# Kernel tuning notes

Hardware: AMD Instinct MI355X
Metric: run time of the kernel (lower is better)

The kernel has to match this reference:

```python
import jax, jax.numpy as jnp
import numpy as np


def conv1d_same(x, w, b, dilation=1):
    # x: [B, T, Cin], w: [K, Cin, Cout] (WIO), 'same' padding, stride 1
    y = jax.lax.conv_general_dilated(
        x, w, window_strides=(1,), padding='SAME',
        rhs_dilation=(dilation,), dimension_numbers=('NWC', 'WIO', 'NWC'))
    return y + b


def setup_inputs() -> dict:
    key = jax.random.key(0)
    ks = jax.random.split(key, 6)
    B, T, N_IN, N_OUT, ATTN_DIM, KSZ = 16, 2048, 96, 128, 64, 3
    return {
        'x': jax.random.normal(ks[0], (B, T, N_IN), jnp.float32),
        'qkv_w': jax.random.normal(ks[1], (N_IN, 3 * ATTN_DIM), jnp.float32) * 0.05,
        'qkv_b': jnp.zeros((3 * ATTN_DIM,), jnp.float32),
        'scale': jnp.ones((), jnp.float32),
        'conv_w1': jax.random.normal(ks[2], (KSZ, ATTN_DIM, N_OUT), jnp.float32) * 0.05,
        'conv_b1': jnp.zeros((N_OUT,), jnp.float32),
        'conv_w2': jax.random.normal(ks[3], (KSZ, N_OUT, N_OUT), jnp.float32) * 0.05,
        'conv_b2': jnp.zeros((N_OUT,), jnp.float32),
        'down_w': jax.random.normal(ks[4], (N_IN, N_OUT), jnp.float32) * 0.1,
    }


def reference(x, qkv_w, qkv_b, scale, conv_w1, conv_b1, conv_w2, conv_b2, down_w):
    # Dense4Attention: single Dense(3*attn_dim), split into q,k,v
    qkv = x @ qkv_w + qkv_b                       # [B,T,3*D]
    q, k, v = jnp.split(qkv, 3, axis=-1)          # each [B,T,D]
    # AttentionBlock: scores = q k^T * learned scale; non-causal (default)
    scores = jnp.einsum('btd,bsd->bts', q, k) * scale   # [B,T,T]
    weights = jax.nn.softmax(scores, axis=2)            # softmax_axis=2
    out_attn = jnp.einsum('bts,bsd->btd', weights, v)   # [B,T,D]
    h = jax.nn.relu(conv1d_same(out_attn, conv_w1, conv_b1, 1))
    out = jax.nn.relu(conv1d_same(h, conv_w2, conv_b2, 1))   # [B,T,n_out]
    # enhanced residual: softmax over time of row-sums of attn weights
    weight_x = jax.nn.softmax(jnp.sum(weights, axis=2), axis=1)  # [B,T]
    en_res_x = (weight_x[..., None] * x) @ down_w   # n_in != n_out -> downsample
    res = x @ down_w                                 # skip path downsample
    return jax.nn.relu(out + res + en_res_x)
```

## Files before the change

kernel.cpp:

```cpp
#include <hip/hip_runtime.h>
#include <cstdint>

#define B_   16
#define T_   2048
#define CIN  96
#define DH   64
#define NOUT 128

typedef float floatx4 __attribute__((ext_vector_type(4)));
typedef short shortx8 __attribute__((ext_vector_type(8)));
typedef unsigned int uintx2 __attribute__((ext_vector_type(2)));

__device__ __forceinline__ unsigned short f2bf(float f) {
  unsigned int u = __float_as_uint(f);
  u += 0x7FFFu + ((u >> 16) & 1u);
  return (unsigned short)(u >> 16);
}
__device__ __forceinline__ uint32_t cvtpk(float lo, float hi) {
  uint32_t r;
  asm("v_cvt_pk_bf16_f32 %0, %1, %2" : "=v"(r) : "v"(lo), "v"(hi));
  return r;
}
__device__ __forceinline__ floatx4 f4zero() { floatx4 v; v[0]=0.f;v[1]=0.f;v[2]=0.f;v[3]=0.f; return v; }
__device__ __forceinline__ shortx8 s8zero() { shortx8 v;
#pragma unroll
  for (int i=0;i<8;++i) v[i]=0; return v; }

__device__ __forceinline__ void plane_swap(uint32_t& a, uint32_t& b) {
#if __has_builtin(__builtin_amdgcn_permlane32_swap) && __has_builtin(__builtin_amdgcn_permlane16_swap)
  uintx2 r1 = __builtin_amdgcn_permlane32_swap(a, b, false, false);
  uintx2 r2 = __builtin_amdgcn_permlane16_swap(r1[0], r1[1], false, false);
  a = r2[0]; b = r2[1];
#else
  asm volatile("v_permlane32_swap_b32 %0, %1\n\t"
               "v_permlane16_swap_b32 %0, %1"
               : "+v"(a), "+v"(b));
#endif
}

__global__ __launch_bounds__(256) void k_wprep(
    const float* __restrict__ qkv_w, const float* __restrict__ cw1,
    const float* __restrict__ cw2, const float* __restrict__ dw,
    unsigned short* __restrict__ qwt, unsigned short* __restrict__ w1t,
    unsigned short* __restrict__ w2t, unsigned short* __restrict__ dwt)
{
  int o = blockIdx.x * 256 + threadIdx.x;
  if (o < 18432) {
    int co = o / 96, ci = o % 96;
    qwt[o] = f2bf(qkv_w[ci * 192 + co]);
  } else if (o < 43008) {
    int p = o - 18432;
    int tap = p / 8192, rem = p % 8192, co = rem >> 6, ci = rem & 63;
    w1t[p] = f2bf(cw1[(tap * 64 + ci) * 128 + co]);
  } else if (o < 92160) {
    int p = o - 43008;
    int tap = p / 16384, rem = p % 16384, co = rem >> 7, ci = rem & 127;
    w2t[p] = f2bf(cw2[(tap * 128 + ci) * 128 + co]);
  } else if (o < 104448) {
    int p = o - 92160;
    int co = p / 96, ci = p % 96;
    dwt[p] = f2bf(dw[ci * 128 + co]);
  }
}

__global__ __launch_bounds__(256) void k_qkv(
    const float* __restrict__ x, const unsigned short* __restrict__ qwt,
    const float* __restrict__ qkv_b, const float* __restrict__ scale_p,
    unsigned short* __restrict__ qb, unsigned short* __restrict__ kb,
    unsigned short* __restrict__ vT)
{
  __shared__ __align__(16) unsigned short Xs[64][104];
  __shared__ __align__(16) unsigned short Vs[64][72];
  const int bx = blockIdx.x;
  const int b = bx >> 5, t0 = (bx & 31) * 64;
  const int tid = threadIdx.x, wave = tid >> 6, lane = tid & 63;
  const int l15 = lane & 15, quad = lane >> 4;
  const float scl2 = scale_p[0] * 1.4426950408889634f;

  for (int idx = tid; idx < 64 * 24; idx += 256) {
    int r = idx / 24, c = (idx % 24) * 4;
    float4 xv = *(const float4*)(x + ((size_t)(b * T_ + t0 + r)) * CIN + c);
    ushort4 o; o.x = f2bf(xv.x); o.y = f2bf(xv.y); o.z = f2bf(xv.z); o.w = f2bf(xv.w);
    *(ushort4*)(&Xs[r][c]) = o;
  }
  __syncthreads();

  floatx4 acc[4][3];
#pragma unroll
  for (int mt = 0; mt < 4; ++mt)
#pragma unroll
    for (int nt = 0; nt < 3; ++nt) acc[mt][nt] = f4zero();

#pragma unroll
  for (int ks = 0; ks < 3; ++ks) {
    shortx8 wf[3];
#pragma unroll
    for (int nt = 0; nt < 3; ++nt) {
      int j = wave * 48 + nt * 16 + l15;
      wf[nt] = *(const shortx8*)(qwt + (size_t)j * 96 + ks * 32 + quad * 8);
    }
#pragma unroll
    for (int mt = 0; mt < 4; ++mt) {
      shortx8 af = *(const shortx8*)(&Xs[mt * 16 + l15][ks * 32 + quad * 8]);
#pragma unroll
      for (int nt = 0; nt < 3; ++nt)
        acc[mt][nt] = __builtin_amdgcn_mfma_f32_16x16x32_bf16(af, wf[nt], acc[mt][nt], 0, 0, 0);
    }
  }

#pragma unroll
  for (int nt = 0; nt < 3; ++nt) {
    int j0 = wave * 48 + nt * 16;
    int j = j0 + l15;
    float bias = qkv_b[j];
#pragma unroll
    for (int mt = 0; mt < 4; ++mt) {
#pragma unroll
      for (int r = 0; r < 4; ++r) {
        int t = t0 + mt * 16 + quad * 4 + r;
        float v = acc[mt][nt][r] + bias;
        if (j0 < 64)        qb[((size_t)b * T_ + t) * DH + j] = f2bf(v * scl2);
        else if (j0 < 128)  kb[((size_t)b * T_ + t) * DH + (j - 64)] = f2bf(v);
        else                Vs[j - 128][mt * 16 + quad * 4 + r] = f2bf(v);
      }
    }
  }
  __syncthreads();
  for (int idx = tid; idx < 64 * 8; idx += 256) {
    int d = idx >> 3, seg = (idx & 7) * 8;
    *(shortx8*)(vT + ((size_t)b * DH + d) * T_ + t0 + seg) =
        *(const shortx8*)(&Vs[d][seg]);
  }
}

__global__ __launch_bounds__(256) void k_attn(
    const unsigned short* __restrict__ qb, const unsigned short* __restrict__ kb,
    const unsigned short* __restrict__ vT,
    unsigned short* __restrict__ ab)
{
  __shared__ __align__(16) unsigned short Kt[64][72];
  __shared__ __align__(16) unsigned short Vt[80][72];
  const int bx = blockIdx.x;
  const int qt = bx & 31, b = bx >> 5;
  const int tid = threadIdx.x, wave = tid >> 6, lane = tid & 63;
  const int l15 = lane & 15, quad = lane >> 4;

  const unsigned short* qrow = qb + ((size_t)b * T_ + qt * 64 + wave * 16 + l15) * DH;
  shortx8 qf0 = *(const shortx8*)(qrow + quad * 8);
  shortx8 qf1 = *(const shortx8*)(qrow + 32 + quad * 8);

  floatx4 O[5];
#pragma unroll
  for (int i = 0; i < 5; ++i) O[i] = f4zero();

  const unsigned short* kbase = kb + (size_t)b * T_ * DH;
  const unsigned short* vbase = vT + (size_t)b * DH * T_;

  for (int idx = tid; idx < 16 * 72; idx += 256) {
    int r = idx / 72, c = idx % 72;
    Vt[64 + r][c] = (r == 0) ? (unsigned short)0x3F80 : (unsigned short)0;
  }

  const int kr0 = tid >> 3, kc = (tid & 7) * 8;
  shortx8 pk[2], pv[2];
#pragma unroll
  for (int i = 0; i < 2; ++i) {
    pk[i] = *(const shortx8*)(kbase + (size_t)(kr0 + i * 32) * DH + kc);
    pv[i] = *(const shortx8*)(vbase + (size_t)(kr0 + i * 32) * T_ + kc);
  }

  for (int t = 0; t < 32; ++t) {
#pragma unroll
    for (int i = 0; i < 2; ++i) {
      *(shortx8*)(&Kt[kr0 + i * 32][kc]) = pk[i];
      *(shortx8*)(&Vt[kr0 + i * 32][kc]) = pv[i];
    }
    __syncthreads();

    if (t < 31) {
      int s0 = (t + 1) * 64;
#pragma unroll
      for (int i = 0; i < 2; ++i) {
        pk[i] = *(const shortx8*)(kbase + (size_t)(s0 + kr0 + i * 32) * DH + kc);
        pv[i] = *(const shortx8*)(vbase + (size_t)(kr0 + i * 32) * T_ + s0 + kc);
      }
    }

    floatx4 S[4];
#pragma unroll
    for (int nt = 0; nt < 4; ++nt) {
      shortx8 bk0 = *(const shortx8*)(&Kt[nt * 16 + l15][quad * 8]);
      shortx8 bk1 = *(const shortx8*)(&Kt[nt * 16 + l15][32 + quad * 8]);
      S[nt] = f4zero();
      S[nt] = __builtin_amdgcn_mfma_f32_16x16x32_bf16(bk0, qf0, S[nt], 0, 0, 0);
      S[nt] = __builtin_amdgcn_mfma_f32_16x16x32_bf16(bk1, qf1, S[nt], 0, 0, 0);
    }

    uint32_t pkv[8];
#pragma unroll
    for (int nt = 0; nt < 4; ++nt) {
#pragma unroll
      for (int j = 0; j < 2; ++j)
        pkv[nt * 2 + j] = cvtpk(exp2f(S[nt][2 * j]), exp2f(S[nt][2 * j + 1]));
    }

#pragma unroll
    for (int kk = 0; kk < 2; ++kk) {
      uint32_t a0 = pkv[4 * kk + 0], b0 = pkv[4 * kk + 2];
      plane_swap(a0, b0);
      uint32_t a1 = pkv[4 * kk + 1], b1 = pkv[4 * kk + 3];
      plane_swap(a1, b1);
      union { shortx8 s; uint32_t u[4]; } fu;
      fu.u[0] = a0; fu.u[1] = a1; fu.u[2] = b0; fu.u[3] = b1;
#pragma unroll
      for (int dt = 0; dt < 5; ++dt) {
        shortx8 bv = *(const shortx8*)(&Vt[dt * 16 + l15][kk * 32 + quad * 8]);
        O[dt] = __builtin_amdgcn_mfma_f32_16x16x32_bf16(fu.s, bv, O[dt], 0, 0, 0);
      }
    }
    __syncthreads();
  }

  unsigned short* abase = ab + ((size_t)b * T_ + qt * 64 + wave * 16) * DH;
#pragma unroll
  for (int r = 0; r < 4; ++r) {
    float s = __shfl(O[4][r], quad << 4);
    float inv = 1.f / s;
    int row = quad * 4 + r;
#pragma unroll
    for (int dt = 0; dt < 4; ++dt)
      abase[(size_t)row * DH + dt * 16 + l15] = f2bf(O[dt][r] * inv);
  }
}

__global__ __launch_bounds__(256) void k_conv1(
    const unsigned short* __restrict__ ab, const unsigned short* __restrict__ w1t,
    const float* __restrict__ b1, unsigned short* __restrict__ hb)
{
  __shared__ __align__(16) unsigned short At[66][72];
  const int bx = blockIdx.x;
  const int b = bx >> 5, t0 = (bx & 31) * 64;
  const int tid = threadIdx.x, wave = tid >> 6, lane = tid & 63;
  const int l15 = lane & 15, quad = lane >> 4;

  for (int idx = tid; idx < 66 * 8; idx += 256) {
    int r = idx >> 3, c = (idx & 7) * 8;
    int t = t0 + r - 1;
    shortx8 v = s8zero();
    if (t >= 0 && t < T_) v = *(const shortx8*)(ab + ((size_t)b * T_ + t) * DH + c);
    *(shortx8*)(&At[r][c]) = v;
  }
  __syncthreads();

  floatx4 acc[4][2];
#pragma unroll
  for (int mt = 0; mt < 4; ++mt) { acc[mt][0] = f4zero(); acc[mt][1] = f4zero(); }

#pragma unroll
  for (int tap = 0; tap < 3; ++tap) {
#pragma unroll
    for (int ks = 0; ks < 2; ++ks) {
      shortx8 wf[2];
#pragma unroll
      for (int ct = 0; ct < 2; ++ct) {
        int co = wave * 32 + ct * 16 + l15;
        wf[ct] = *(const shortx8*)(w1t + ((size_t)tap * 128 + co) * 64 + ks * 32 + quad * 8);
      }
#pragma unroll
      for (int mt = 0; mt < 4; ++mt) {
        shortx8 af = *(const shortx8*)(&At[mt * 16 + l15 + tap][ks * 32 + quad * 8]);
        acc[mt][0] = __builtin_amdgcn_mfma_f32_16x16x32_bf16(af, wf[0], acc[mt][0], 0, 0, 0);
        acc[mt][1] = __builtin_amdgcn_mfma_f32_16x16x32_bf16(af, wf[1], acc[mt][1], 0, 0, 0);
      }
    }
  }

#pragma unroll
  for (int ct = 0; ct < 2; ++ct) {
    int co = wave * 32 + ct * 16 + l15;
    float bias = b1[co];
#pragma unroll
    for (int mt = 0; mt < 4; ++mt)
#pragma unroll
      for (int r = 0; r < 4; ++r) {
        int t = t0 + mt * 16 + quad * 4 + r;
        hb[((size_t)b * T_ + t) * NOUT + co] = f2bf(fmaxf(acc[mt][ct][r] + bias, 0.f));
      }
  }
}

__global__ __launch_bounds__(256) void k_conv2(
    const unsigned short* __restrict__ hb, const float* __restrict__ x,
    const unsigned short* __restrict__ w2t, const unsigned short* __restrict__ dwt,
    const float* __restrict__ b2, float* __restrict__ out)
{
  __shared__ __align__(16) unsigned short Ht[66][136];
  __shared__ __align__(16) unsigned short Xt[64][104];
  const int bx = blockIdx.x;
  const int b = bx >> 5, t0 = (bx & 31) * 64;
  const int tid = threadIdx.x, wave = tid >> 6, lane = tid & 63;
  const int l15 = lane & 15, quad = lane >> 4;

  for (int idx = tid; idx < 66 * 16; idx += 256) {
    int r = idx >> 4, c = (idx & 15) * 8;
    int t = t0 + r - 1;
    shortx8 v = s8zero();
    if (t >= 0 && t < T_) v = *(const shortx8*)(hb + ((size_t)b * T_ + t) * NOUT + c);
    *(shortx8*)(&Ht[r][c]) = v;
  }
  for (int idx = tid; idx < 64 * 24; idx += 256) {
    int r = idx / 24, c = (idx % 24) * 4;
    float4 xv = *(const float4*)(x + ((size_t)(b * T_ + t0 + r)) * CIN + c);
    ushort4 o; o.x = f2bf(xv.x); o.y = f2bf(xv.y); o.z = f2bf(xv.z); o.w = f2bf(xv.w);
    *(ushort4*)(&Xt[r][c]) = o;
  }
  __syncthreads();

  floatx4 a2[4][2], ar[4][2];
#pragma unroll
  for (int mt = 0; mt < 4; ++mt) { a2[mt][0]=f4zero(); a2[mt][1]=f4zero(); ar[mt][0]=f4zero(); ar[mt][1]=f4zero(); }

#pragma unroll
  for (int tap = 0; tap < 3; ++tap) {
#pragma unroll
    for (int ks = 0; ks < 4; ++ks) {
      shortx8 wf[2];
#pragma unroll
      for (int ct = 0; ct < 2; ++ct) {
        int co = wave * 32 + ct * 16 + l15;
        wf[ct] = *(const shortx8*)(w2t + ((size_t)tap * 128 + co) * 128 + ks * 32 + quad * 8);
      }
#pragma unroll
      for (int mt = 0; mt < 4; ++mt) {
        shortx8 af = *(const shortx8*)(&Ht[mt * 16 + l15 + tap][ks * 32 + quad * 8]);
        a2[mt][0] = __builtin_amdgcn_mfma_f32_16x16x32_bf16(af, wf[0], a2[mt][0], 0, 0, 0);
        a2[mt][1] = __builtin_amdgcn_mfma_f32_16x16x32_bf16(af, wf[1], a2[mt][1], 0, 0, 0);
      }
    }
  }
#pragma unroll
  for (int ks = 0; ks < 3; ++ks) {
    shortx8 wf[2];
#pragma unroll
    for (int ct = 0; ct < 2; ++ct) {
      int co = wave * 32 + ct * 16 + l15;
      wf[ct] = *(const shortx8*)(dwt + (size_t)co * 96 + ks * 32 + quad * 8);
    }
#pragma unroll
    for (int mt = 0; mt < 4; ++mt) {
      shortx8 af = *(const shortx8*)(&Xt[mt * 16 + l15][ks * 32 + quad * 8]);
      ar[mt][0] = __builtin_amdgcn_mfma_f32_16x16x32_bf16(af, wf[0], ar[mt][0], 0, 0, 0);
      ar[mt][1] = __builtin_amdgcn_mfma_f32_16x16x32_bf16(af, wf[1], ar[mt][1], 0, 0, 0);
    }
  }

  const float kres = 1.0f + 1.0f / 2048.0f;
#pragma unroll
  for (int ct = 0; ct < 2; ++ct) {
    int co = wave * 32 + ct * 16 + l15;
    float bias = b2[co];
#pragma unroll
    for (int mt = 0; mt < 4; ++mt)
#pragma unroll
      for (int r = 0; r < 4; ++r) {
        int t = t0 + mt * 16 + quad * 4 + r;
        float o2 = fmaxf(a2[mt][ct][r] + bias, 0.f);
        out[((size_t)b * T_ + t) * NOUT + co] = fmaxf(o2 + ar[mt][ct][r] * kres, 0.f);
      }
  }
}

extern "C" void kernel_launch(void* const* d_in, const int* in_sizes, int n_in,
                              void* d_out, int out_size, void* d_ws, size_t ws_size,
                              hipStream_t stream) {
  const float* x      = (const float*)d_in[0];
  const float* qkv_w  = (const float*)d_in[1];
  const float* qkv_b  = (const float*)d_in[2];
  const float* scale  = (const float*)d_in[3];
  const float* cw1    = (const float*)d_in[4];
  const float* cb1    = (const float*)d_in[5];
  const float* cw2    = (const float*)d_in[6];
  const float* cb2    = (const float*)d_in[7];
  const float* dw     = (const float*)d_in[8];

  char* ws = (char*)d_ws;
  unsigned short* qb  = (unsigned short*)(ws + 0);
  unsigned short* kb  = (unsigned short*)(ws + 4194304);
  unsigned short* vT  = (unsigned short*)(ws + 8388608);
  unsigned short* ab  = (unsigned short*)(ws + 12582912);
  unsigned short* hb  = (unsigned short*)(ws + 16777216);
  unsigned short* qwt = (unsigned short*)(ws + 25165824);
  unsigned short* w1t = (unsigned short*)(ws + 25202688);
  unsigned short* w2t = (unsigned short*)(ws + 25251840);
  unsigned short* dwt = (unsigned short*)(ws + 25350144);

  k_wprep<<<408, 256, 0, stream>>>(qkv_w, cw1, cw2, dw, qwt, w1t, w2t, dwt);
  k_qkv  <<<512, 256, 0, stream>>>(x, qwt, qkv_b, scale, qb, kb, vT);
  k_attn <<<512, 256, 0, stream>>>(qb, kb, vT, ab);
  k_conv1<<<512, 256, 0, stream>>>(ab, w1t, cb1, hb);
  k_conv2<<<512, 256, 0, stream>>>(hb, x, w2t, dwt, cb2, (float*)d_out);
}
```

Before: 146.4 us.

## Fuse conv1 and conv2 into one kernel with halo recompute in shared memory

Measured after the change: 143.2 us. -2.2%, faster.

```diff
diff --git a/kernel.cpp b/kernel.cpp
--- a/kernel.cpp
+++ b/kernel.cpp
@@ -233,80 +233,27 @@
   }
 }
 
-__global__ __launch_bounds__(256) void k_conv1(
-    const unsigned short* __restrict__ ab, const unsigned short* __restrict__ w1t,
-    const float* __restrict__ b1, unsigned short* __restrict__ hb)
+__global__ __launch_bounds__(256) void k_conv12(
+    const unsigned short* __restrict__ ab, const float* __restrict__ x,
+    const unsigned short* __restrict__ w1t, const unsigned short* __restrict__ w2t,
+    const unsigned short* __restrict__ dwt,
+    const float* __restrict__ b1, const float* __restrict__ b2,
+    float* __restrict__ out)
 {
-  __shared__ __align__(16) unsigned short At[66][72];
-  const int bx = blockIdx.x;
-  const int b = bx >> 5, t0 = (bx & 31) * 64;
-  const int tid = threadIdx.x, wave = tid >> 6, lane = tid & 63;
-  const int l15 = lane & 15, quad = lane >> 4;
-
-  for (int idx = tid; idx < 66 * 8; idx += 256) {
-    int r = idx >> 3, c = (idx & 7) * 8;
-    int t = t0 + r - 1;
-    shortx8 v = s8zero();
-    if (t >= 0 && t < T_) v = *(const shortx8*)(ab + ((size_t)b * T_ + t) * DH + c);
-    *(shortx8*)(&At[r][c]) = v;
-  }
-  __syncthreads();
-
-  floatx4 acc[4][2];
-#pragma unroll
-  for (int mt = 0; mt < 4; ++mt) { acc[mt][0] = f4zero(); acc[mt][1] = f4zero(); }
-
-#pragma unroll
-  for (int tap = 0; tap < 3; ++tap) {
-#pragma unroll
-    for (int ks = 0; ks < 2; ++ks) {
-      shortx8 wf[2];
-#pragma unroll
-      for (int ct = 0; ct < 2; ++ct) {
-        int co = wave * 32 + ct * 16 + l15;
-        wf[ct] = *(const shortx8*)(w1t + ((size_t)tap * 128 + co) * 64 + ks * 32 + quad * 8);
-      }
-#pragma unroll
-      for (int mt = 0; mt < 4; ++mt) {
-        shortx8 af = *(const shortx8*)(&At[mt * 16 + l15 + tap][ks * 32 + quad * 8]);
-        acc[mt][0] = __builtin_amdgcn_mfma_f32_16x16x32_bf16(af, wf[0], acc[mt][0], 0, 0, 0);
-        acc[mt][1] = __builtin_amdgcn_mfma_f32_16x16x32_bf16(af, wf[1], acc[mt][1], 0, 0, 0);
-      }
-    }
-  }
-
-#pragma unroll
-  for (int ct = 0; ct < 2; ++ct) {
-    int co = wave * 32 + ct * 16 + l15;
-    float bias = b1[co];
-#pragma unroll
-    for (int mt = 0; mt < 4; ++mt)
-#pragma unroll
-      for (int r = 0; r < 4; ++r) {
-        int t = t0 + mt * 16 + quad * 4 + r;
-        hb[((size_t)b * T_ + t) * NOUT + co] = f2bf(fmaxf(acc[mt][ct][r] + bias, 0.f));
-      }
-  }
-}
-
-__global__ __launch_bounds__(256) void k_conv2(
-    const unsigned short* __restrict__ hb, const float* __restrict__ x,
-    const unsigned short* __restrict__ w2t, const unsigned short* __restrict__ dwt,
-    const float* __restrict__ b2, float* __restrict__ out)
-{
-  __shared__ __align__(16) unsigned short Ht[66][136];
+  __shared__ __align__(16) unsigned short At[82][72];
+  __shared__ __align__(16) unsigned short Ht[80][136];
   __shared__ __align__(16) unsigned short Xt[64][104];
   const int bx = blockIdx.x;
   const int b = bx >> 5, t0 = (bx & 31) * 64;
   const int tid = threadIdx.x, wave = tid >> 6, lane = tid & 63;
   const int l15 = lane & 15, quad = lane >> 4;
 
-  for (int idx = tid; idx < 66 * 16; idx += 256) {
-    int r = idx >> 4, c = (idx & 15) * 8;
-    int t = t0 + r - 1;
+  for (int idx = tid; idx < 82 * 8; idx += 256) {
+    int r = idx >> 3, c = (idx & 7) * 8;
+    int t = t0 + r - 9;
     shortx8 v = s8zero();
-    if (t >= 0 && t < T_) v = *(const shortx8*)(hb + ((size_t)b * T_ + t) * NOUT + c);
-    *(shortx8*)(&Ht[r][c]) = v;
+    if (t >= 0 && t < T_) v = *(const shortx8*)(ab + ((size_t)b * T_ + t) * DH + c);
+    *(shortx8*)(&At[r][c]) = v;
   }
   for (int idx = tid; idx < 64 * 24; idx += 256) {
     int r = idx / 24, c = (idx % 24) * 4;
@@ -316,6 +263,48 @@
   }
   __syncthreads();
 
+  {
+    floatx4 acc[5][2];
+#pragma unroll
+    for (int mt = 0; mt < 5; ++mt) { acc[mt][0] = f4zero(); acc[mt][1] = f4zero(); }
+
+#pragma unroll
+    for (int tap = 0; tap < 3; ++tap) {
+#pragma unroll
+      for (int ks = 0; ks < 2; ++ks) {
+        shortx8 wf[2];
+#pragma unroll
+        for (int ct = 0; ct < 2; ++ct) {
+          int co = wave * 32 + ct * 16 + l15;
+          wf[ct] = *(const shortx8*)(w1t + ((size_t)tap * 128 + co) * 64 + ks * 32 + quad * 8);
+        }
+#pragma unroll
+        for (int mt = 0; mt < 5; ++mt) {
+          shortx8 af = *(const shortx8*)(&At[mt * 16 + l15 + tap][ks * 32 + quad * 8]);
+          acc[mt][0] = __builtin_amdgcn_mfma_f32_16x16x32_bf16(af, wf[0], acc[mt][0], 0, 0, 0);
+          acc[mt][1] = __builtin_amdgcn_mfma_f32_16x16x32_bf16(af, wf[1], acc[mt][1], 0, 0, 0);
+        }
+      }
+    }
+
+#pragma unroll
+    for (int ct = 0; ct < 2; ++ct) {
+      int co = wave * 32 + ct * 16 + l15;
+      float bias = b1[co];
+#pragma unroll
+      for (int mt = 0; mt < 5; ++mt)
+#pragma unroll
+        for (int r = 0; r < 4; ++r) {
+          int hr = mt * 16 + quad * 4 + r;
+          int t = t0 - 8 + hr;
+          unsigned short hv = 0;
+          if (t >= 0 && t < T_) hv = f2bf(fmaxf(acc[mt][ct][r] + bias, 0.f));
+          Ht[hr][co] = hv;
+        }
+    }
+  }
+  __syncthreads();
+
   floatx4 a2[4][2], ar[4][2];
 #pragma unroll
   for (int mt = 0; mt < 4; ++mt) { a2[mt][0]=f4zero(); a2[mt][1]=f4zero(); ar[mt][0]=f4zero(); ar[mt][1]=f4zero(); }
@@ -332,7 +321,7 @@
       }
 #pragma unroll
       for (int mt = 0; mt < 4; ++mt) {
-        shortx8 af = *(const shortx8*)(&Ht[mt * 16 + l15 + tap][ks * 32 + quad * 8]);
+        shortx8 af = *(const shortx8*)(&Ht[mt * 16 + l15 + 7 + tap][ks * 32 + quad * 8]);
         a2[mt][0] = __builtin_amdgcn_mfma_f32_16x16x32_bf16(af, wf[0], a2[mt][0], 0, 0, 0);
         a2[mt][1] = __builtin_amdgcn_mfma_f32_16x16x32_bf16(af, wf[1], a2[mt][1], 0, 0, 0);
       }
@@ -388,15 +377,13 @@
   unsigned short* kb  = (unsigned short*)(ws + 4194304);
   unsigned short* vT  = (unsigned short*)(ws + 8388608);
   unsigned short* ab  = (unsigned short*)(ws + 12582912);
-  unsigned short* hb  = (unsigned short*)(ws + 16777216);
   unsigned short* qwt = (unsigned short*)(ws + 25165824);
   unsigned short* w1t = (unsigned short*)(ws + 25202688);
   unsigned short* w2t = (unsigned short*)(ws + 25251840);
   unsigned short* dwt = (unsigned short*)(ws + 25350144);
 
-  k_wprep<<<408, 256, 0, stream>>>(qkv_w, cw1, cw2, dw, qwt, w1t, w2t, dwt);
-  k_qkv  <<<512, 256, 0, stream>>>(x, qwt, qkv_b, scale, qb, kb, vT);
-  k_attn <<<512, 256, 0, stream>>>(qb, kb, vT, ab);
-  k_conv1<<<512, 256, 0, stream>>>(ab, w1t, cb1, hb);
-  k_conv2<<<512, 256, 0, stream>>>(hb, x, w2t, dwt, cb2, (float*)d_out);
-}
+  k_wprep <<<408, 256, 0, stream>>>(qkv_w, cw1, cw2, dw, qwt, w1t, w2t, dwt);
+  k_qkv   <<<512, 256, 0, stream>>>(x, qwt, qkv_b, scale, qb, kb, vT);
+  k_attn  <<<512, 256, 0, stream>>>(qb, kb, vT, ab);
+  k_conv12<<<512, 256, 0, stream>>>(ab, x, w1t, w2t, dwt, cb1, cb2, (float*)d_out);
+}
```
